# Kernel optimization log

Measured on AMD Instinct MI355X. Metric: run time of the kernel, lower is better.

Reference implementation:

```python
import jax, jax.numpy as jnp
import numpy as np

# S6Layer dims: d_model=256; internal d_state=max(8,16//2)=8; expand=max(1.5,2*0.75)=1.5 -> d_inner=384
B, L, DM = 8, 4096, 256
DI, DS = 384, 8
CHUNK = 32  # seq_len > 64 path: chunked scan, state resets to 0 at every chunk (faithful to source)
EPS = 1e-5


def setup_inputs() -> dict:
    key = jax.random.key(0)
    ks = jax.random.split(key, 8)
    def w(k, shape, s=0.02):
        return jax.random.normal(k, shape, jnp.float32) * s
    return {
        "x": jax.random.normal(ks[0], (B, L, DM), jnp.float32),
        "gamma": jnp.ones((DM,), jnp.float32),
        "beta": jnp.zeros((DM,), jnp.float32),
        "W_in": w(ks[1], (3 * DI, DM)),
        "b_in": jnp.zeros((3 * DI,), jnp.float32),
        "W_dt": w(ks[2], (DI, DI)),
        "b_dt": jnp.zeros((DI,), jnp.float32),
        "A_log": jax.random.normal(ks[3], (DI, DS), jnp.float32),
        "D_vec": jax.random.normal(ks[4], (DI,), jnp.float32),
        "W_out": w(ks[5], (DM, DI)),
        "b_out": jnp.zeros((DM,), jnp.float32),
    }


def _layernorm(x, g, b):
    mu = jnp.mean(x, axis=-1, keepdims=True)
    var = jnp.mean(jnp.square(x - mu), axis=-1, keepdims=True)
    return (x - mu) * jax.lax.rsqrt(var + EPS) * g + b


def _chunked_scan(xp, dt, A):
    # xp, dt: [B, L, DI]; A: [DI, DS]. Each CHUNK-length block scans from h=0
    # (the torch code never propagates h across chunks for seq_len > 64).
    C = L // CHUNK
    xr = xp.reshape(B, C, CHUNK, DI)
    dtr = dt.reshape(B, C, CHUNK, DI)
    dA = jnp.exp(dtr[..., None] * A)              # [B, C, T, DI, DS]
    dA_t = jnp.moveaxis(dA, 2, 0)                 # [T, B, C, DI, DS]
    x_t = jnp.moveaxis(xr, 2, 0)                  # [T, B, C, DI]

    def step(h, inp):
        dA_i, x_i = inp
        h = h * dA_i + x_i[..., None]             # broadcast x over DS
        return h, jnp.sum(h, axis=-1)             # y_i: [B, C, DI]

    h0 = jnp.zeros((B, C, DI, DS), xp.dtype)
    _, ys = jax.lax.scan(step, h0, (dA_t, x_t))   # ys: [T, B, C, DI]
    return jnp.moveaxis(ys, 0, 2).reshape(B, L, DI)


def reference(x, gamma, beta, W_in, b_in, W_dt, b_dt, A_log, D_vec, W_out, b_out):
    residual = x
    xn = _layernorm(x, gamma, beta)
    xz = xn @ W_in.T + b_in                       # [B, L, 3*DI]
    x_proj, z, dt_in = jnp.split(xz, 3, axis=-1)
    x_proj = jax.nn.silu(x_proj)
    z = jax.nn.silu(z)
    dt = jax.nn.softplus(dt_in @ W_dt.T + b_dt)   # [B, L, DI]
    A = -jnp.exp(A_log)                           # [DI, DS]
    y = _chunked_scan(x_proj, dt, A)
    y = y * z + x_proj * D_vec
    return y @ W_out.T + b_out + residual
```

## Files before the change

kernel.cpp:

```cpp
#include <hip/hip_runtime.h>
#include <stdint.h>

#define B_  8
#define L_  4096
#define DM  256
#define DI  384
#define DS  8
#define M_  (B_*L_)

typedef float f32x4 __attribute__((ext_vector_type(4)));
typedef short s16x8 __attribute__((ext_vector_type(8)));

#define AS1(p) ((__attribute__((address_space(1))) void*)(p))
#define AS3(p) ((__attribute__((address_space(3))) void*)(p))

__device__ __forceinline__ unsigned short f2bf(float f) {
  union { float f; uint32_t u; } v; v.f = f;
  uint32_t r = v.u + 0x7FFFu + ((v.u >> 16) & 1u);
  return (unsigned short)(r >> 16);
}
__device__ __forceinline__ float bf2f(unsigned short h) {
  union { uint32_t u; float f; } v; v.u = ((uint32_t)h) << 16;
  return v.f;
}
__device__ __forceinline__ float silu_f(float x) {
  return x * __builtin_amdgcn_rcpf(1.f + __expf(-x));
}

__global__ __launch_bounds__(256) void cvt_kernel(
    const float* __restrict__ w0, const float* __restrict__ w1, const float* __restrict__ w2,
    unsigned short* __restrict__ o0, unsigned short* __restrict__ o1, unsigned short* __restrict__ o2) {
  int i = blockIdx.x * 256 + threadIdx.x;
  if (i < 3*DI*DM) o0[i] = f2bf(w0[i]);
  if (i < DI*DI)   o1[i] = f2bf(w1[i]);
  if (i < DM*DI)   o2[i] = f2bf(w2[i]);
}

__global__ __launch_bounds__(256) void ln_kernel(
    const float* __restrict__ x, const float* __restrict__ gamma, const float* __restrict__ beta,
    unsigned short* __restrict__ xn) {
  int token = blockIdx.x * 4 + (threadIdx.x >> 6);
  int lane  = threadIdx.x & 63;
  const float4 v = *(const float4*)(x + (size_t)token*DM + lane*4);
  float s  = v.x + v.y + v.z + v.w;
  float ss = v.x*v.x + v.y*v.y + v.z*v.z + v.w*v.w;
  #pragma unroll
  for (int off = 32; off > 0; off >>= 1) {
    s  += __shfl_xor(s,  off, 64);
    ss += __shfl_xor(ss, off, 64);
  }
  float mean = s * (1.f/DM);
  float var  = ss * (1.f/DM) - mean*mean;
  float rstd = rsqrtf(var + 1e-5f);
  const float4 g = *(const float4*)(gamma + lane*4);
  const float4 b = *(const float4*)(beta  + lane*4);
  ushort4 o;
  o.x = f2bf((v.x - mean)*rstd*g.x + b.x);
  o.y = f2bf((v.y - mean)*rstd*g.y + b.y);
  o.z = f2bf((v.z - mean)*rstd*g.z + b.z);
  o.w = f2bf((v.w - mean)*rstd*g.w + b.w);
  *(ushort4*)(xn + (size_t)token*DM + lane*4) = o;
}

template<int EPI, int KSTEPS>
__global__ __launch_bounds__(256, 3) void gemm_ws(
    const unsigned short* __restrict__ A,
    const unsigned short* __restrict__ Bw,
    const float* __restrict__ bias,
    unsigned short* __restrict__ o_xp, unsigned short* __restrict__ o_z,
    unsigned short* __restrict__ o_dtin,
    unsigned short* __restrict__ o_bf,
    const float* __restrict__ resid, float* __restrict__ o_f)
{
  constexpr int K    = KSTEPS * 32;
  constexpr int CPR  = K / 8;
  constexpr int PF   = (KSTEPS < 8) ? KSTEPS : 8;
  __shared__ unsigned short smem[64*K];
  unsigned short* sB = smem;

  const int t    = threadIdx.x;
  const int lane = t & 63;
  const int w    = t >> 6;
  const int fr   = lane & 15;
  const int fq   = lane >> 4;
  const int mbase = blockIdx.x * 128;
  const int nbase = blockIdx.y * 64;
  const int wm   = w * 32;

  #pragma unroll
  for (int i = 0; i < (64*CPR)/256; ++i) {
    int c   = i*256 + t;
    int row = c / CPR;
    int j   = c - row*CPR;
    int jp  = (j & ~7) | ((j & 7) ^ (row & 7));
    __builtin_amdgcn_global_load_lds(AS1(Bw + (size_t)(nbase + row)*K + jp*8),
                                     AS3(sB + c*8), 16, 0, 0);
  }

  const unsigned short* gA0 = A + (size_t)(mbase + wm + fr)*K + fq*8;
  const unsigned short* gA1 = gA0 + (size_t)16*K;

  s16x8 af[PF][2];
  #pragma unroll
  for (int p = 0; p < PF; ++p) {
    af[p][0] = *(const s16x8*)(gA0 + p*32);
    af[p][1] = *(const s16x8*)(gA1 + p*32);
  }
  __builtin_amdgcn_sched_barrier(0);

  const unsigned short* sBrE = sB + (size_t)fr*K + ( fq      ^ (fr & 7))*8;
  const unsigned short* sBrO = sB + (size_t)fr*K + ((fq | 4) ^ (fr & 7))*8;

  f32x4 acc[2][4];
  #pragma unroll
  for (int mi = 0; mi < 2; ++mi)
    #pragma unroll
    for (int ni = 0; ni < 4; ++ni) acc[mi][ni] = (f32x4){0.f, 0.f, 0.f, 0.f};

  __syncthreads();

  #pragma unroll
  for (int kt = 0; kt < KSTEPS; ++kt) {
    s16x8 a0 = af[kt % PF][0];
    s16x8 a1 = af[kt % PF][1];
    if (kt + PF < KSTEPS) {
      af[kt % PF][0] = *(const s16x8*)(gA0 + (kt + PF)*32);
      af[kt % PF][1] = *(const s16x8*)(gA1 + (kt + PF)*32);
    }
    const unsigned short* bb = (kt & 1) ? sBrO : sBrE;
    s16x8 bfr[4];
    #pragma unroll
    for (int ni = 0; ni < 4; ++ni)
      bfr[ni] = *(const s16x8*)(bb + ni*16*K + (kt >> 1)*64);
    #pragma unroll
    for (int ni = 0; ni < 4; ++ni) {
      acc[0][ni] = __builtin_amdgcn_mfma_f32_16x16x32_bf16(a0, bfr[ni], acc[0][ni], 0, 0, 0);
      acc[1][ni] = __builtin_amdgcn_mfma_f32_16x16x32_bf16(a1, bfr[ni], acc[1][ni], 0, 0, 0);
    }
  }

  if constexpr (EPI == 3) {
    #pragma unroll
    for (int ni = 0; ni < 4; ++ni) {
      int gn = nbase + ni*16 + fr;
      float bv = bias[gn];
      #pragma unroll
      for (int mi = 0; mi < 2; ++mi) {
        int gm0 = mbase + wm + mi*16 + fq*4;
        #pragma unroll
        for (int r = 0; r < 4; ++r) {
          size_t gm = (size_t)(gm0 + r);
          o_f[gm*DM + gn] = acc[mi][ni][r] + bv + resid[gm*DM + gn];
        }
      }
    }
  } else {
    __syncthreads();
    const bool do_silu = (EPI == 1) && (blockIdx.y < 12);
    #pragma unroll
    for (int ni = 0; ni < 4; ++ni) {
      int cn = ni*16 + fr;
      float bv = bias[nbase + cn];
      #pragma unroll
      for (int mi = 0; mi < 2; ++mi) {
        int rm0 = wm + mi*16 + fq*4;
        #pragma unroll
        for (int r = 0; r < 4; ++r) {
          float c = acc[mi][ni][r] + bv;
          if constexpr (EPI == 1) { if (do_silu) c = silu_f(c); }
          else                    { c = (c > 20.f) ? c : __logf(1.f + __expf(c)); }
          smem[(rm0 + r)*72 + cn] = f2bf(c);
        }
      }
    }
    __syncthreads();
    unsigned short* dst;
    int colbase;
    if constexpr (EPI == 1) {
      int p = blockIdx.y;
      dst = (p < 6) ? o_xp : (p < 12) ? o_z : o_dtin;
      colbase = (p % 6) * 64;
    } else {
      dst = o_bf; colbase = nbase;
    }
    const int rr = t >> 3, cc = (t & 7) * 8;
    #pragma unroll
    for (int it = 0; it < 4; ++it) {
      int row = rr + it*32;
      s16x8 v = *(const s16x8*)(smem + row*72 + cc);
      *(s16x8*)(dst + (size_t)(mbase + row)*DI + colbase + cc) = v;
    }
  }
}

__global__ __launch_bounds__(384) void scan_kernel(
    const unsigned short* __restrict__ xp, const unsigned short* __restrict__ dt,
    const unsigned short* __restrict__ zb, const float* __restrict__ A_log,
    const float* __restrict__ D_vec, unsigned short* __restrict__ yz) {
  int g  = blockIdx.x;
  int di = threadIdx.x;
  size_t base = (size_t)g * 32 * DI + di;
  float a[DS];
  #pragma unroll
  for (int s = 0; s < DS; ++s) a[s] = -__expf(A_log[di*DS + s]);
  float Dv = D_vec[di];
  float h[DS] = {0.f,0.f,0.f,0.f,0.f,0.f,0.f,0.f};
  for (int tt = 0; tt < 32; ++tt) {
    size_t idx = base + (size_t)tt * DI;
    float xv  = bf2f(xp[idx]);
    float dtv = bf2f(dt[idx]);
    float y = 0.f;
    #pragma unroll
    for (int s = 0; s < DS; ++s) {
      h[s] = h[s] * __expf(dtv * a[s]) + xv;
      y += h[s];
    }
    float zv = bf2f(zb[idx]);
    yz[idx] = f2bf(y * zv + xv * Dv);
  }
}

extern "C" void kernel_launch(void* const* d_in, const int* in_sizes, int n_in,
                              void* d_out, int out_size, void* d_ws, size_t ws_size,
                              hipStream_t stream) {
  const float* x     = (const float*)d_in[0];
  const float* gamma = (const float*)d_in[1];
  const float* beta  = (const float*)d_in[2];
  const float* W_in  = (const float*)d_in[3];
  const float* b_in  = (const float*)d_in[4];
  const float* W_dt  = (const float*)d_in[5];
  const float* b_dt  = (const float*)d_in[6];
  const float* A_log = (const float*)d_in[7];
  const float* D_vec = (const float*)d_in[8];
  const float* W_out = (const float*)d_in[9];
  const float* b_out = (const float*)d_in[10];
  float* out = (float*)d_out;

  char* ws = (char*)d_ws;
  size_t off = 0;
  auto alloc = [&](size_t bytes) -> char* {
    char* p = ws + off; off += (bytes + 255) & ~(size_t)255; return p;
  };
  unsigned short* xn    = (unsigned short*)alloc((size_t)M_*DM*2);
  unsigned short* xpb   = (unsigned short*)alloc((size_t)M_*DI*2);
  unsigned short* zb    = (unsigned short*)alloc((size_t)M_*DI*2);
  unsigned short* dtin  = (unsigned short*)alloc((size_t)M_*DI*2);
  unsigned short* dtb   = (unsigned short*)alloc((size_t)M_*DI*2);
  unsigned short* yzb   = dtin;
  unsigned short* winb  = (unsigned short*)alloc((size_t)3*DI*DM*2);
  unsigned short* wdtb  = (unsigned short*)alloc((size_t)DI*DI*2);
  unsigned short* woutb = (unsigned short*)alloc((size_t)DM*DI*2);

  cvt_kernel<<<dim3((3*DI*DM + 255)/256), 256, 0, stream>>>(W_in, W_dt, W_out, winb, wdtb, woutb);
  ln_kernel<<<dim3(M_/4), 256, 0, stream>>>(x, gamma, beta, xn);
  gemm_ws<1, 8><<<dim3(M_/128, (3*DI)/64), 256, 0, stream>>>(
      xn, winb, b_in, xpb, zb, dtin, nullptr, nullptr, nullptr);
  gemm_ws<2, 12><<<dim3(M_/128, DI/64), 256, 0, stream>>>(
      dtin, wdtb, b_dt, nullptr, nullptr, nullptr, dtb, nullptr, nullptr);
  scan_kernel<<<dim3(M_/32), DI, 0, stream>>>(xpb, dtb, zb, A_log, D_vec, yzb);
  gemm_ws<3, 12><<<dim3(M_/128, DM/64), 256, 0, stream>>>(
      yzb, woutb, b_out, nullptr, nullptr, nullptr, nullptr, x, out);
}
```

Baseline: 239.9 us.

## Process two M-tiles per GEMM block with swizzled grid and per-wave epilogue

```diff
diff --git a/kernel.cpp b/kernel.cpp
--- a/kernel.cpp
+++ b/kernel.cpp
@@ -62,7 +62,7 @@
   *(ushort4*)(xn + (size_t)token*DM + lane*4) = o;
 }
 
-template<int EPI, int KSTEPS>
+template<int EPI, int KSTEPS, int MT>
 __global__ __launch_bounds__(256, 3) void gemm_ws(
     const unsigned short* __restrict__ A,
     const unsigned short* __restrict__ Bw,
@@ -74,18 +74,21 @@
 {
   constexpr int K    = KSTEPS * 32;
   constexpr int CPR  = K / 8;
-  constexpr int PF   = (KSTEPS < 8) ? KSTEPS : 8;
-  __shared__ unsigned short smem[64*K];
-  unsigned short* sB = smem;
+  __shared__ unsigned short sB[64*K];
+  __shared__ unsigned short sC[(EPI == 3) ? 2 : 4*32*72];
 
   const int t    = threadIdx.x;
   const int lane = t & 63;
   const int w    = t >> 6;
   const int fr   = lane & 15;
   const int fq   = lane >> 4;
-  const int mbase = blockIdx.x * 128;
-  const int nbase = blockIdx.y * 64;
   const int wm   = w * 32;
+
+  const int q    = blockIdx.y * 128 + blockIdx.x;
+  const int bx2  = (q & 7) * 16 + ((q >> 3) & 15);
+  const int by2  = q >> 7;
+  const int mbase0 = bx2 * (128 * MT);
+  const int nbase  = by2 * 64;
 
   #pragma unroll
   for (int i = 0; i < (64*CPR)/256; ++i) {
@@ -97,98 +100,92 @@
                                      AS3(sB + c*8), 16, 0, 0);
   }
 
-  const unsigned short* gA0 = A + (size_t)(mbase + wm + fr)*K + fq*8;
-  const unsigned short* gA1 = gA0 + (size_t)16*K;
-
-  s16x8 af[PF][2];
-  #pragma unroll
-  for (int p = 0; p < PF; ++p) {
-    af[p][0] = *(const s16x8*)(gA0 + p*32);
-    af[p][1] = *(const s16x8*)(gA1 + p*32);
-  }
-  __builtin_amdgcn_sched_barrier(0);
-
   const unsigned short* sBrE = sB + (size_t)fr*K + ( fq      ^ (fr & 7))*8;
   const unsigned short* sBrO = sB + (size_t)fr*K + ((fq | 4) ^ (fr & 7))*8;
 
-  f32x4 acc[2][4];
-  #pragma unroll
-  for (int mi = 0; mi < 2; ++mi)
+  float bvv[4];
+  #pragma unroll
+  for (int ni = 0; ni < 4; ++ni) bvv[ni] = bias[nbase + ni*16 + fr];
+
+  unsigned short* sCw = sC + w*(32*72);
+
+  __syncthreads();
+
+  #pragma unroll
+  for (int mt = 0; mt < MT; ++mt) {
+    const int mbase = mbase0 + mt*128;
+    const unsigned short* gA0 = A + (size_t)(mbase + wm + fr)*K + fq*8;
+    const unsigned short* gA1 = gA0 + (size_t)16*K;
+
+    f32x4 acc[2][4];
     #pragma unroll
-    for (int ni = 0; ni < 4; ++ni) acc[mi][ni] = (f32x4){0.f, 0.f, 0.f, 0.f};
-
-  __syncthreads();
-
-  #pragma unroll
-  for (int kt = 0; kt < KSTEPS; ++kt) {
-    s16x8 a0 = af[kt % PF][0];
-    s16x8 a1 = af[kt % PF][1];
-    if (kt + PF < KSTEPS) {
-      af[kt % PF][0] = *(const s16x8*)(gA0 + (kt + PF)*32);
-      af[kt % PF][1] = *(const s16x8*)(gA1 + (kt + PF)*32);
+    for (int mi = 0; mi < 2; ++mi)
+      #pragma unroll
+      for (int ni = 0; ni < 4; ++ni) acc[mi][ni] = (f32x4){0.f, 0.f, 0.f, 0.f};
+
+    #pragma unroll
+    for (int kt = 0; kt < KSTEPS; ++kt) {
+      s16x8 a0 = *(const s16x8*)(gA0 + kt*32);
+      s16x8 a1 = *(const s16x8*)(gA1 + kt*32);
+      const unsigned short* bb = (kt & 1) ? sBrO : sBrE;
+      s16x8 bfr[4];
+      #pragma unroll
+      for (int ni = 0; ni < 4; ++ni)
+        bfr[ni] = *(const s16x8*)(bb + ni*16*K + (kt >> 1)*64);
+      #pragma unroll
+      for (int ni = 0; ni < 4; ++ni) {
+        acc[0][ni] = __builtin_amdgcn_mfma_f32_16x16x32_bf16(a0, bfr[ni], acc[0][ni], 0, 0, 0);
+        acc[1][ni] = __builtin_amdgcn_mfma_f32_16x16x32_bf16(a1, bfr[ni], acc[1][ni], 0, 0, 0);
+      }
     }
-    const unsigned short* bb = (kt & 1) ? sBrO : sBrE;
-    s16x8 bfr[4];
-    #pragma unroll
-    for (int ni = 0; ni < 4; ++ni)
-      bfr[ni] = *(const s16x8*)(bb + ni*16*K + (kt >> 1)*64);
-    #pragma unroll
-    for (int ni = 0; ni < 4; ++ni) {
-      acc[0][ni] = __builtin_amdgcn_mfma_f32_16x16x32_bf16(a0, bfr[ni], acc[0][ni], 0, 0, 0);
-      acc[1][ni] = __builtin_amdgcn_mfma_f32_16x16x32_bf16(a1, bfr[ni], acc[1][ni], 0, 0, 0);
-    }
-  }
-
-  if constexpr (EPI == 3) {
-    #pragma unroll
-    for (int ni = 0; ni < 4; ++ni) {
-      int gn = nbase + ni*16 + fr;
-      float bv = bias[gn];
-      #pragma unroll
-      for (int mi = 0; mi < 2; ++mi) {
-        int gm0 = mbase + wm + mi*16 + fq*4;
+
+    if constexpr (EPI == 3) {
+      #pragma unroll
+      for (int ni = 0; ni < 4; ++ni) {
+        int gn = nbase + ni*16 + fr;
         #pragma unroll
-        for (int r = 0; r < 4; ++r) {
-          size_t gm = (size_t)(gm0 + r);
-          o_f[gm*DM + gn] = acc[mi][ni][r] + bv + resid[gm*DM + gn];
+        for (int mi = 0; mi < 2; ++mi) {
+          int gm0 = mbase + wm + mi*16 + fq*4;
+          #pragma unroll
+          for (int r = 0; r < 4; ++r) {
+            size_t gm = (size_t)(gm0 + r);
+            o_f[gm*DM + gn] = acc[mi][ni][r] + bvv[ni] + resid[gm*DM + gn];
+          }
         }
       }
-    }
-  } else {
-    __syncthreads();
-    const bool do_silu = (EPI == 1) && (blockIdx.y < 12);
-    #pragma unroll
-    for (int ni = 0; ni < 4; ++ni) {
-      int cn = ni*16 + fr;
-      float bv = bias[nbase + cn];
-      #pragma unroll
-      for (int mi = 0; mi < 2; ++mi) {
-        int rm0 = wm + mi*16 + fq*4;
+    } else {
+      const bool do_silu = (EPI == 1) && (by2 < 12);
+      #pragma unroll
+      for (int ni = 0; ni < 4; ++ni) {
+        int cn = ni*16 + fr;
         #pragma unroll
-        for (int r = 0; r < 4; ++r) {
-          float c = acc[mi][ni][r] + bv;
-          if constexpr (EPI == 1) { if (do_silu) c = silu_f(c); }
-          else                    { c = (c > 20.f) ? c : __logf(1.f + __expf(c)); }
-          smem[(rm0 + r)*72 + cn] = f2bf(c);
+        for (int mi = 0; mi < 2; ++mi) {
+          int rm0 = mi*16 + fq*4;
+          #pragma unroll
+          for (int r = 0; r < 4; ++r) {
+            float c = acc[mi][ni][r] + bvv[ni];
+            if constexpr (EPI == 1) { if (do_silu) c = silu_f(c); }
+            else                    { c = (c > 20.f) ? c : __logf(1.f + __expf(c)); }
+            sCw[(rm0 + r)*72 + cn] = f2bf(c);
+          }
         }
       }
-    }
-    __syncthreads();
-    unsigned short* dst;
-    int colbase;
-    if constexpr (EPI == 1) {
-      int p = blockIdx.y;
-      dst = (p < 6) ? o_xp : (p < 12) ? o_z : o_dtin;
-      colbase = (p % 6) * 64;
-    } else {
-      dst = o_bf; colbase = nbase;
-    }
-    const int rr = t >> 3, cc = (t & 7) * 8;
-    #pragma unroll
-    for (int it = 0; it < 4; ++it) {
-      int row = rr + it*32;
-      s16x8 v = *(const s16x8*)(smem + row*72 + cc);
-      *(s16x8*)(dst + (size_t)(mbase + row)*DI + colbase + cc) = v;
+      asm volatile("s_waitcnt lgkmcnt(0)" ::: "memory");
+      unsigned short* dst;
+      int colbase;
+      if constexpr (EPI == 1) {
+        dst = (by2 < 6) ? o_xp : (by2 < 12) ? o_z : o_dtin;
+        colbase = (by2 % 6) * 64;
+      } else {
+        dst = o_bf; colbase = nbase;
+      }
+      const int rr = lane >> 3, cc = (lane & 7) * 8;
+      #pragma unroll
+      for (int it = 0; it < 4; ++it) {
+        int row32 = rr + it*8;
+        s16x8 v = *(const s16x8*)(sCw + row32*72 + cc);
+        *(s16x8*)(dst + (size_t)(mbase + wm + row32)*DI + colbase + cc) = v;
+      }
     }
   }
 }
@@ -253,11 +250,11 @@
 
   cvt_kernel<<<dim3((3*DI*DM + 255)/256), 256, 0, stream>>>(W_in, W_dt, W_out, winb, wdtb, woutb);
   ln_kernel<<<dim3(M_/4), 256, 0, stream>>>(x, gamma, beta, xn);
-  gemm_ws<1, 8><<<dim3(M_/128, (3*DI)/64), 256, 0, stream>>>(
+  gemm_ws<1, 8, 2><<<dim3(128, (3*DI)/64), 256, 0, stream>>>(
       xn, winb, b_in, xpb, zb, dtin, nullptr, nullptr, nullptr);
-  gemm_ws<2, 12><<<dim3(M_/128, DI/64), 256, 0, stream>>>(
+  gemm_ws<2, 12, 2><<<dim3(128, DI/64), 256, 0, stream>>>(
       dtin, wdtb, b_dt, nullptr, nullptr, nullptr, dtb, nullptr, nullptr);
   scan_kernel<<<dim3(M_/32), DI, 0, stream>>>(xpb, dtb, zb, A_log, D_vec, yzb);
-  gemm_ws<3, 12><<<dim3(M_/128, DM/64), 256, 0, stream>>>(
+  gemm_ws<3, 12, 2><<<dim3(128, DM/64), 256, 0, stream>>>(
       yzb, woutb, b_out, nullptr, nullptr, nullptr, nullptr, x, out);
 }
```

Result: faster. 224.2 us (-6.5%).
